# Kernel optimization log

Measured on AMD Instinct MI355X. Metric: run time of the kernel, lower is better.

## Reference

```python
import jax, jax.numpy as jnp
import numpy as np

D, H, L, FF, IN, OUT, S, B = 512, 8, 6, 2048, 32, 3, 512, 32


def setup_inputs() -> dict:
    key = jax.random.key(0)
    ks = iter(jax.random.split(key, 32))
    w = lambda shape: jax.random.normal(next(ks), shape, jnp.float32) * 0.02
    z = lambda shape: jnp.zeros(shape, jnp.float32)
    o = lambda shape: jnp.ones(shape, jnp.float32)
    return {
        'x': jax.random.normal(next(ks), (B, S, IN), jnp.float32),
        'w_in': w((IN, D)), 'b_in': z((D,)), 'g_in': o((D,)), 'be_in': z((D,)),
        'w_qkv': w((L, D, 3 * D)), 'b_qkv': z((L, 3 * D)),
        'w_out': w((L, D, D)), 'b_out': z((L, D)),
        'g1': o((L, D)), 'be1': z((L, D)),
        'w_ff1': w((L, D, FF)), 'b_ff1': z((L, FF)),
        'w_ff2': w((L, FF, D)), 'b_ff2': z((L, D)),
        'g2': o((L, D)), 'be2': z((L, D)),
        'w_h1': w((D, D // 2)), 'b_h1': z((D // 2,)),
        'w_h2': w((D // 2, OUT)), 'b_h2': z((OUT,)),
    }


def _layer_norm(x, g, b, eps=1e-5):
    mu = jnp.mean(x, axis=-1, keepdims=True)
    var = jnp.mean(jnp.square(x - mu), axis=-1, keepdims=True)
    return (x - mu) / jnp.sqrt(var + eps) * g + b


def _gelu(x):
    return jax.nn.gelu(x, approximate=False)  # torch nn.GELU default (erf)


def _pos_encoding(seq_len, d_model):
    pos = jnp.arange(seq_len, dtype=jnp.float32)[:, None]
    div = jnp.exp(jnp.arange(0, d_model, 2, dtype=jnp.float32) * (-np.log(10000.0) / d_model))
    pe = jnp.zeros((seq_len, d_model), jnp.float32)
    pe = pe.at[:, 0::2].set(jnp.sin(pos * div))
    pe = pe.at[:, 1::2].set(jnp.cos(pos * div))
    return pe


def reference(x, w_in, b_in, g_in, be_in, w_qkv, b_qkv, w_out, b_out,
              g1, be1, w_ff1, b_ff1, w_ff2, b_ff2, g2, be2,
              w_h1, b_h1, w_h2, b_h2):
    b, s, _ = x.shape
    d = w_in.shape[1]
    hd = d // H
    scale = hd ** -0.5

    # input projection: Linear -> LayerNorm -> GELU (dropout = identity at eval)
    h = _gelu(_layer_norm(x @ w_in + b_in, g_in, be_in))
    h = h + _pos_encoding(s, d)

    causal_mask = jnp.triu(jnp.ones((s, s), bool), 1)  # True above diagonal = future

    for l in range(w_qkv.shape[0]):
        qkv = (h @ w_qkv[l] + b_qkv[l]).reshape(b, s, 3, H, hd)
        q, k, v = qkv[:, :, 0], qkv[:, :, 1], qkv[:, :, 2]  # [b, s, H, hd]
        scores = jnp.einsum('bihd,bjhd->bhij', q, k) * scale
        scores = jnp.where(causal_mask, -jnp.inf, scores)
        attn = jax.nn.softmax(scores, axis=-1)
        o = jnp.einsum('bhij,bjhd->bihd', attn, v).reshape(b, s, d)
        o = o @ w_out[l] + b_out[l]
        h = _layer_norm(h + o, g1[l], be1[l])
        f = _gelu(h @ w_ff1[l] + b_ff1[l]) @ w_ff2[l] + b_ff2[l]
        h = _layer_norm(h + f, g2[l], be2[l])

    logits = _gelu(h @ w_h1 + b_h1) @ w_h2 + b_h2  # [b, s, OUT]
    return logits[:, -1, :]  # last position only
```

## Files before the change

### kernel.cpp

```cpp
#include <hip/hip_runtime.h>
#include <hip/hip_bf16.h>
#include <math.h>

#define D_   512
#define H_   8
#define HD_  64
#define L_   6
#define FF_  2048
#define IN_  32
#define OUT_ 3
#define S_   512
#define B_   32
#define M_   (B_ * S_)

typedef __attribute__((ext_vector_type(8))) short short8;
typedef __attribute__((ext_vector_type(4))) float floatx4;

__device__ __forceinline__ float gelu_f(float x) {
    const float ax = fabsf(x) * 0.70710678118654752f;
    const float t = __builtin_amdgcn_rcpf(fmaf(0.3275911f, ax, 1.0f));
    float p = fmaf(1.061405429f, t, -1.453152027f);
    p = fmaf(p, t, 1.421413741f);
    p = fmaf(p, t, -0.284496736f);
    p = fmaf(p, t, 0.254829592f);
    p = p * t;
    const float e = __expf(-ax * ax);
    const float er = copysignf(fmaf(-p, e, 1.0f), x);
    return 0.5f * x * (1.0f + er);
}
__device__ __forceinline__ float bf2f(unsigned short u) {
    union { unsigned int i; float f; } c; c.i = ((unsigned)u) << 16; return c.f;
}
__device__ __forceinline__ unsigned short f2bf(float v) {
    __hip_bfloat16 t = __float2bfloat16(v);
    return *(unsigned short*)&t;
}
__device__ __forceinline__ void async16(const void* g, void* l) {
    __builtin_amdgcn_global_load_lds(
        (const __attribute__((address_space(1))) unsigned int*)g,
        (__attribute__((address_space(3))) unsigned int*)l, 16, 0, 0);
}
__device__ __forceinline__ void stage2(const short* g, char* d, long rs, int off2) {
    async16(g, d);
    async16(g + rs, d + off2);
}


template<int DO_GELU, int OUT_BF16, int ADD_RES>
__global__ __launch_bounds__(256, 2)
void gemm_mfma_k(const __hip_bfloat16* __restrict__ A,
                 const __hip_bfloat16* __restrict__ WT,
                 const float* __restrict__ bias,
                 const float* __restrict__ R,
                 void* __restrict__ C,
                 int N, int K) {
    __shared__ __align__(16) char smem[65536];
    float* Ep = (float*)smem;

    const int tid  = threadIdx.x;
    const int lane = tid & 63;
    const int wave = tid >> 6;

    const int Lid = blockIdx.y * gridDim.x + blockIdx.x;
    const int xcd = Lid & 7;
    const int idx = Lid >> 3;
    const int gx  = gridDim.x, gy8 = gridDim.y >> 3;
    const int m0 = (xcd * gy8 + idx / gx) * 128;
    const int n0 = (idx % gx) * 128;

    const int wm = (wave >> 1) * 64, wn = (wave & 1) * 64;
    const int r = lane & 15, q = lane >> 4;
    const int qa = (q ^ ((r >> 1) & 3)) * 8;

    const int srow = tid >> 2;
    const int sc = ((tid & 3) ^ ((tid >> 3) & 3)) * 8;
    const short* Ag = (const short*)A + (long)(m0 + srow) * K + sc;
    const short* Bg = (const short*)WT + (long)(n0 + srow) * K + sc;
    const long rs = (long)64 * K;

    floatx4 acc[4][4];
    #pragma unroll
    for (int i = 0; i < 4; i++)
        #pragma unroll
        for (int j = 0; j < 4; j++) acc[i][j] = (floatx4)0.f;

    const int NT = K >> 6;

    stage2(Ag,      smem + 0     + tid * 16, rs, 4096);
    stage2(Bg,      smem + 16384 + tid * 16, rs, 4096);
    stage2(Ag + 32, smem + 8192  + tid * 16, rs, 4096);
    stage2(Bg + 32, smem + 24576 + tid * 16, rs, 4096);
    asm volatile("s_waitcnt vmcnt(4)" ::: "memory");
    __builtin_amdgcn_s_barrier();
    __builtin_amdgcn_sched_barrier(0);

    short8 a[4], b[4];
    for (int t = 0; t < NT; ++t) {
        const int cur = t & 1, nxt = cur ^ 1;
        const bool hn = (t + 1 < NT);
        const short* As = (const short*)(smem + cur * 32768);
        const short* Bs = (const short*)(smem + cur * 32768 + 16384);
        const short* Agt = Ag + (t + 1) * 64;
        const short* Bgt = Bg + (t + 1) * 64;
        char* Ad = smem + nxt * 32768;
        char* Bd = smem + nxt * 32768 + 16384;

        if (hn) {
            stage2(Agt, Ad + tid * 16, rs, 4096);
            stage2(Bgt, Bd + tid * 16, rs, 4096);
        }
        #pragma unroll
        for (int i = 0; i < 4; i++)
            a[i] = *(const short8*)&As[(wm + i * 16 + r) * 32 + qa];
        #pragma unroll
        for (int j = 0; j < 4; j++)
            b[j] = *(const short8*)&Bs[(wn + j * 16 + r) * 32 + qa];
        #pragma unroll
        for (int i = 0; i < 4; i++)
            #pragma unroll
            for (int j = 0; j < 4; j++)
                acc[i][j] = __builtin_amdgcn_mfma_f32_16x16x32_bf16(
                    a[i], b[j], acc[i][j], 0, 0, 0);
        __builtin_amdgcn_sched_barrier(0);
        if (hn) asm volatile("s_waitcnt vmcnt(4)" ::: "memory");
        else    asm volatile("s_waitcnt vmcnt(0)" ::: "memory");
        __builtin_amdgcn_s_barrier();
        __builtin_amdgcn_sched_barrier(0);

        if (hn) {
            stage2(Agt + 32, Ad + 8192 + tid * 16, rs, 4096);
            stage2(Bgt + 32, Bd + 8192 + tid * 16, rs, 4096);
        }
        #pragma unroll
        for (int i = 0; i < 4; i++)
            a[i] = *(const short8*)&As[4096 + (wm + i * 16 + r) * 32 + qa];
        #pragma unroll
        for (int j = 0; j < 4; j++)
            b[j] = *(const short8*)&Bs[4096 + (wn + j * 16 + r) * 32 + qa];
        #pragma unroll
        for (int i = 0; i < 4; i++)
            #pragma unroll
            for (int j = 0; j < 4; j++)
                acc[i][j] = __builtin_amdgcn_mfma_f32_16x16x32_bf16(
                    a[i], b[j], acc[i][j], 0, 0, 0);
        __builtin_amdgcn_sched_barrier(0);
        if (hn) asm volatile("s_waitcnt vmcnt(4)" ::: "memory");
        __builtin_amdgcn_s_barrier();
        __builtin_amdgcn_sched_barrier(0);
    }

    const int erow = tid >> 5;
    const int ecol = (tid & 31) * 4;
    const float4 bvec = *(const float4*)&bias[n0 + ecol];

    #pragma unroll
    for (int pass = 0; pass < 2; pass++) {
        if (pass) __syncthreads();
        if ((wave >> 1) == pass) {
            #pragma unroll
            for (int i = 0; i < 4; i++)
                #pragma unroll
                for (int j = 0; j < 4; j++)
                    #pragma unroll
                    for (int rg = 0; rg < 4; rg++)
                        Ep[(i * 16 + q * 4 + rg) * 132 + wn + j * 16 + r] =
                            acc[i][j][rg];
        }
        __syncthreads();
        #pragma unroll
        for (int it = 0; it < 8; it++) {
            const int row = it * 8 + erow;
            const long grow = (long)(m0 + pass * 64 + row) * N + n0 + ecol;
            const float4 v = *(const float4*)&Ep[row * 132 + ecol];
            float o0 = v.x + bvec.x, o1 = v.y + bvec.y;
            float o2 = v.z + bvec.z, o3 = v.w + bvec.w;
            if (DO_GELU) {
                o0 = gelu_f(o0); o1 = gelu_f(o1);
                o2 = gelu_f(o2); o3 = gelu_f(o3);
            }
            if (ADD_RES) {
                const float4 rv = *(const float4*)&R[grow];
                o0 += rv.x; o1 += rv.y; o2 += rv.z; o3 += rv.w;
            }
            if (OUT_BF16) {
                ushort4 pk;
                pk.x = f2bf(o0); pk.y = f2bf(o1);
                pk.z = f2bf(o2); pk.w = f2bf(o3);
                *(ushort4*)((unsigned short*)C + grow) = pk;
            } else {
                *(float4*)((float*)C + grow) = make_float4(o0, o1, o2, o3);
            }
        }
    }
}

__global__ __launch_bounds__(512, 1)
void gemm_ln_k(const __hip_bfloat16* __restrict__ A,
               const __hip_bfloat16* __restrict__ WT,
               const float* __restrict__ bias,
               const float* R,
               const float* __restrict__ g,
               const float* __restrict__ be,
               float* Hout,
               __hip_bfloat16* __restrict__ Hb,
               int K) {
    __shared__ __align__(16) char smem[147456];
    const int tid  = threadIdx.x;
    const int lane = tid & 63;
    const int wave = tid >> 6;

    const int Lid = blockIdx.x;
    const int m0 = ((Lid & 7) * 32 + (Lid >> 3)) * 64;

    const int r = lane & 15, q = lane >> 4;
    const int qaB  = (q ^ ((r >> 1) & 3)) * 8;
    const int qaA0 = ((q)     ^ (r & 7)) * 8;
    const int qaA1 = ((4 + q) ^ (r & 7)) * 8;
    const int wn = wave * 64;

    const int arow = tid >> 3;
    const int asb  = ((tid & 7) ^ ((tid >> 3) & 7)) * 8;
    const short* Ag = (const short*)A + (long)(m0 + arow) * K + asb;
    const int brow = tid >> 2;
    const int bsb  = ((tid & 3) ^ ((tid >> 3) & 3)) * 8;
    const short* Bg = (const short*)WT + (long)brow * K + bsb;
    const long brs = (long)128 * K;

    floatx4 acc[4][4];
    #pragma unroll
    for (int i = 0; i < 4; i++)
        #pragma unroll
        for (int j = 0; j < 4; j++) acc[i][j] = (floatx4)0.f;

    const int NTT = K >> 6;

    {
        char* base = smem;
        async16(Ag, base + tid * 16);
        const short* p0 = Bg;
        char* d0 = base + 8192 + tid * 16;
        async16(p0, d0); async16(p0 + brs, d0 + 8192);
        async16(p0 + 2 * brs, d0 + 16384); async16(p0 + 3 * brs, d0 + 24576);
        const short* p1 = Bg + 32;
        char* d1 = base + 40960 + tid * 16;
        async16(p1, d1); async16(p1 + brs, d1 + 8192);
        async16(p1 + 2 * brs, d1 + 16384); async16(p1 + 3 * brs, d1 + 24576);
    }
    asm volatile("s_waitcnt vmcnt(4)" ::: "memory");
    __builtin_amdgcn_s_barrier();
    __builtin_amdgcn_sched_barrier(0);

    for (int t = 0; t < NTT; ++t) {
        const int cur = t & 1, nxt = cur ^ 1;
        const bool hn = (t + 1 < NTT);
        const short* As  = (const short*)(smem + cur * 73728);
        const short* B0s = (const short*)(smem + cur * 73728 + 8192);
        const short* B1s = (const short*)(smem + cur * 73728 + 40960);
        char* nb = smem + nxt * 73728;
        const long k1 = (long)(t + 1) * 64;

        if (hn) {
            async16(Ag + k1, nb + tid * 16);
            const short* p0 = Bg + k1;
            char* d0 = nb + 8192 + tid * 16;
            async16(p0, d0); async16(p0 + brs, d0 + 8192);
            async16(p0 + 2 * brs, d0 + 16384); async16(p0 + 3 * brs, d0 + 24576);
        }
        {
            short8 a[4], b[4];
            #pragma unroll
            for (int mf = 0; mf < 4; mf++)
                a[mf] = *(const short8*)&As[(mf * 16 + r) * 64 + qaA0];
            #pragma unroll
            for (int nf = 0; nf < 4; nf++)
                b[nf] = *(const short8*)&B0s[(wn + nf * 16 + r) * 32 + qaB];
            #pragma unroll
            for (int mf = 0; mf < 4; mf++)
                #pragma unroll
                for (int nf = 0; nf < 4; nf++)
                    acc[mf][nf] = __builtin_amdgcn_mfma_f32_16x16x32_bf16(
                        a[mf], b[nf], acc[mf][nf], 0, 0, 0);
        }
        __builtin_amdgcn_sched_barrier(0);
        if (hn) asm volatile("s_waitcnt vmcnt(4)" ::: "memory");
        else    asm volatile("s_waitcnt vmcnt(0)" ::: "memory");
        __builtin_amdgcn_s_barrier();
        __builtin_amdgcn_sched_barrier(0);

        if (hn) {
            const short* p1 = Bg + k1 + 32;
            char* d1 = nb + 40960 + tid * 16;
            async16(p1, d1); async16(p1 + brs, d1 + 8192);
            async16(p1 + 2 * brs, d1 + 16384); async16(p1 + 3 * brs, d1 + 24576);
        }
        {
            short8 a[4], b[4];
            #pragma unroll
            for (int mf = 0; mf < 4; mf++)
                a[mf] = *(const short8*)&As[(mf * 16 + r) * 64 + qaA1];
            #pragma unroll
            for (int nf = 0; nf < 4; nf++)
                b[nf] = *(const short8*)&B1s[(wn + nf * 16 + r) * 32 + qaB];
            #pragma unroll
            for (int mf = 0; mf < 4; mf++)
                #pragma unroll
                for (int nf = 0; nf < 4; nf++)
                    acc[mf][nf] = __builtin_amdgcn_mfma_f32_16x16x32_bf16(
                        a[mf], b[nf], acc[mf][nf], 0, 0, 0);
        }
        __builtin_amdgcn_sched_barrier(0);
        if (hn) asm volatile("s_waitcnt vmcnt(4)" ::: "memory");
        __builtin_amdgcn_s_barrier();
        __builtin_amdgcn_sched_barrier(0);
    }

    float* Ef = (float*)smem;
    float* stat = (float*)(smem + 132096);
    const float gl = g[tid], bl = be[tid], bv = bias[tid];

    #pragma unroll
    for (int mf = 0; mf < 4; mf++)
        #pragma unroll
        for (int nf = 0; nf < 4; nf++)
            #pragma unroll
            for (int rg = 0; rg < 4; rg++)
                Ef[(mf * 16 + q * 4 + rg) * 516 + wn + nf * 16 + r] =
                    acc[mf][nf][rg];
    __syncthreads();
    #pragma unroll 8
    for (int k = 0; k < 64; k++)
        Ef[k * 516 + tid] += bv + R[(long)(m0 + k) * 512 + tid];
    __syncthreads();
    {
        const int row = tid >> 3, cc = tid & 7;
        float s = 0.f, ss = 0.f;
        #pragma unroll 8
        for (int j = 0; j < 64; j++) {
            const float v = Ef[row * 516 + cc + 8 * j];
            s += v; ss += v * v;
        }
        #pragma unroll
        for (int off = 1; off < 8; off <<= 1) {
            s  += __shfl_xor(s, off);
            ss += __shfl_xor(ss, off);
        }
        const float mu  = s * (1.0f / 512.0f);
        const float var = fmaxf(ss * (1.0f / 512.0f) - mu * mu, 0.f);
        const float inv = 1.0f / sqrtf(var + 1e-5f);
        if (cc == 0) { stat[row * 2] = mu; stat[row * 2 + 1] = inv; }
    }
    __syncthreads();
    #pragma unroll 8
    for (int k = 0; k < 64; k++) {
        const float v  = Ef[k * 516 + tid];
        const float o  = (v - stat[k * 2]) * stat[k * 2 + 1] * gl + bl;
        const long idx = (long)(m0 + k) * 512 + tid;
        Hout[idx] = o;
        ((unsigned short*)Hb)[idx] = f2bf(o);
    }
}

__global__ __launch_bounds__(256)
void transpose_cast_k(const float* __restrict__ W, __hip_bfloat16* __restrict__ WT,
                      int K, int N) {
    __shared__ float tile[32][33];
    const float* Wl = W + (long)blockIdx.z * K * N;
    __hip_bfloat16* WTl = WT + (long)blockIdx.z * K * N;
    const int n0 = blockIdx.x * 32, k0 = blockIdx.y * 32;
    const int tx = threadIdx.x & 31, ty = threadIdx.x >> 5;
    for (int rr = ty; rr < 32; rr += 8)
        tile[rr][tx] = Wl[(long)(k0 + rr) * N + n0 + tx];
    __syncthreads();
    for (int rr = ty; rr < 32; rr += 8)
        WTl[(long)(n0 + rr) * K + k0 + tx] = __float2bfloat16(tile[tx][rr]);
}

template<int DO_GELU>
__global__ __launch_bounds__(256)
void gemm_bias_k(const float* __restrict__ A, long lda,
                 const float* __restrict__ W,
                 const float* __restrict__ bias,
                 float* __restrict__ C,
                 int M, int N, int K) {
    __shared__ float As[16][64];
    __shared__ float Ws[16][64];
    const int tx = threadIdx.x;
    const int ty = threadIdx.y;
    const int tid = ty * 16 + tx;
    const int m0 = blockIdx.y * 64;
    const int n0 = blockIdx.x * 64;
    float acc[4][4] = {};
    for (int k0 = 0; k0 < K; k0 += 16) {
        #pragma unroll
        for (int e = tid; e < 64 * 16; e += 256) {
            int m = e >> 4, k = e & 15;
            float v = 0.f;
            if (m0 + m < M) v = A[(long)(m0 + m) * lda + k0 + k];
            As[k][m] = v;
        }
        #pragma unroll
        for (int e = tid; e < 16 * 64; e += 256) {
            int k = e >> 6, n = e & 63;
            float v = 0.f;
            if (n0 + n < N) v = W[(long)(k0 + k) * N + n0 + n];
            Ws[k][n] = v;
        }
        __syncthreads();
        #pragma unroll
        for (int kk = 0; kk < 16; kk++) {
            float a[4], w[4];
            #pragma unroll
            for (int i = 0; i < 4; i++) a[i] = As[kk][ty * 4 + i];
            #pragma unroll
            for (int j = 0; j < 4; j++) w[j] = Ws[kk][tx * 4 + j];
            #pragma unroll
            for (int i = 0; i < 4; i++)
                #pragma unroll
                for (int j = 0; j < 4; j++)
                    acc[i][j] += a[i] * w[j];
        }
        __syncthreads();
    }
    #pragma unroll
    for (int i = 0; i < 4; i++) {
        int m = m0 + ty * 4 + i;
        if (m >= M) continue;
        #pragma unroll
        for (int j = 0; j < 4; j++) {
            int n = n0 + tx * 4 + j;
            if (n >= N) continue;
            float v = acc[i][j] + bias[n];
            if (DO_GELU) v = gelu_f(v);
            C[(long)m * N + n] = v;
        }
    }
}

__global__ __launch_bounds__(256)
void ln_gelu_pos_k(const float* __restrict__ X,
                   const float* __restrict__ g,
                   const float* __restrict__ be,
                   float* __restrict__ Hout,
                   __hip_bfloat16* __restrict__ Hb) {
    const int row = blockIdx.x;
    const int s = row & (S_ - 1);
    const int t = threadIdx.x;
    const float* x = X + (long)row * D_;
    float v0 = x[t], v1 = x[t + 256];
    __shared__ float red[256];
    red[t] = v0 + v1;
    __syncthreads();
    for (int off = 128; off; off >>= 1) {
        if (t < off) red[t] += red[t + off];
        __syncthreads();
    }
    float mu = red[0] * (1.0f / D_);
    __syncthreads();
    float d0 = v0 - mu, d1 = v1 - mu;
    red[t] = d0 * d0 + d1 * d1;
    __syncthreads();
    for (int off = 128; off; off >>= 1) {
        if (t < off) red[t] += red[t + off];
        __syncthreads();
    }
    float var = red[0] * (1.0f / D_);
    float inv = 1.0f / sqrtf(var + 1e-5f);
    float o0 = gelu_f(d0 * inv * g[t] + be[t]);
    float o1 = gelu_f(d1 * inv * g[t + 256] + be[t + 256]);
    {
        int d = t, i = d >> 1;
        float dv = expf((float)(2 * i) * (-9.210340371976184f / 512.0f));
        float ang = (float)s * dv;
        o0 += (d & 1) ? cosf(ang) : sinf(ang);
    }
    {
        int d = t + 256, i = d >> 1;
        float dv = expf((float)(2 * i) * (-9.210340371976184f / 512.0f));
        float ang = (float)s * dv;
        o1 += (d & 1) ? cosf(ang) : sinf(ang);
    }
    Hout[(long)row * D_ + t] = o0;
    Hout[(long)row * D_ + t + 256] = o1;
    Hb[(long)row * D_ + t] = __float2bfloat16(o0);
    Hb[(long)row * D_ + t + 256] = __float2bfloat16(o1);
}

#define LDT 72
__global__ __launch_bounds__(256)
void attn_mfma_k(const __hip_bfloat16* __restrict__ qkv,
                 __hip_bfloat16* __restrict__ O) {
    const int qt = blockIdx.x;
    const int bh = blockIdx.y;
    const int b = bh >> 3, h = bh & (H_ - 1);
    const int tid = threadIdx.x;
    const int wave = tid >> 6, lane = tid & 63;
    const int ln = lane & 15, quad = lane >> 4;
    const int wm = wave * 32;
    const int i0 = qt * 128;

    __shared__ unsigned short Qs[128 * LDT];
    __shared__ unsigned short Ks[64 * LDT];
    __shared__ unsigned short Vt[64 * LDT];
    __shared__ unsigned short Ps[128 * LDT];
    __shared__ float stat[128];

    const unsigned short* base = (const unsigned short*)qkv + (long)b * S_ * (3 * D_);

    {
        const int r0 = tid >> 3, c0 = (tid & 7) * 8;
        #pragma unroll
        for (int i = 0; i < 4; i++) {
            const int rw = i * 32 + r0;
            *(short8*)&Qs[rw * LDT + c0] =
                *(const short8*)(base + (long)(i0 + rw) * (3 * D_) + h * HD_ + c0);
        }
    }

    float m_i[2] = { -INFINITY, -INFINITY };
    float l_i[2] = { 0.f, 0.f };
    floatx4 o_acc[2][4];
    #pragma unroll
    for (int i = 0; i < 2; i++)
        #pragma unroll
        for (int j = 0; j < 4; j++) o_acc[i][j] = (floatx4)0.f;

    const int kr = tid >> 2, kc = (tid & 3) * 16;
    const int vj = tid & 63, vc = (tid >> 6) * 16;

    const int ktmax = 2 * qt + 1;
    for (int kt = 0; kt <= ktmax; kt++) {
        const int j0 = kt * 64;
        {
            const unsigned short* kp = base + (long)(j0 + kr) * (3 * D_) + D_ + h * HD_ + kc;
            *(short8*)&Ks[kr * LDT + kc]     = *(const short8*)(kp);
            *(short8*)&Ks[kr * LDT + kc + 8] = *(const short8*)(kp + 8);
            const unsigned short* vp = base + (long)(j0 + vj) * (3 * D_) + 2 * D_ + h * HD_ + vc;
            short8 v0 = *(const short8*)(vp);
            short8 v1 = *(const short8*)(vp + 8);
            #pragma unroll
            for (int e = 0; e < 8; e++) {
                Vt[(vc + e) * LDT + vj]     = (unsigned short)v0[e];
                Vt[(vc + 8 + e) * LDT + vj] = (unsigned short)v1[e];
            }
        }
        __syncthreads();

        floatx4 sa[4][2];
        #pragma unroll
        for (int mt = 0; mt < 4; mt++)
            #pragma unroll
            for (int nt = 0; nt < 2; nt++) sa[mt][nt] = (floatx4)0.f;
        #pragma unroll
        for (int c = 0; c < 2; c++) {
            short8 kf[4], qf[2];
            #pragma unroll
            for (int mt = 0; mt < 4; mt++)
                kf[mt] = *(const short8*)&Ks[(mt * 16 + ln) * LDT + c * 32 + quad * 8];
            #pragma unroll
            for (int nt = 0; nt < 2; nt++)
                qf[nt] = *(const short8*)&Qs[(wm + nt * 16 + ln) * LDT + c * 32 + quad * 8];
            #pragma unroll
            for (int mt = 0; mt < 4; mt++)
                #pragma unroll
                for (int nt = 0; nt < 2; nt++)
                    sa[mt][nt] = __builtin_amdgcn_mfma_f32_16x16x32_bf16(
                        kf[mt], qf[nt], sa[mt][nt], 0, 0, 0);
        }

        const bool domask = (kt >= 2 * qt);
        #pragma unroll
        for (int nt = 0; nt < 2; nt++) {
            const int qg = i0 + wm + nt * 16 + ln;
            float mx = -INFINITY;
            #pragma unroll
            for (int mt = 0; mt < 4; mt++)
                #pragma unroll
                for (int rg = 0; rg < 4; rg++) {
                    float v = sa[mt][nt][rg] * 0.125f;
                    if (domask && (j0 + mt * 16 + quad * 4 + rg > qg)) v = -INFINITY;
                    sa[mt][nt][rg] = v;
                    mx = fmaxf(mx, v);
                }
            mx = fmaxf(mx, __shfl_xor(mx, 16));
            mx = fmaxf(mx, __shfl_xor(mx, 32));
            const float mn = fmaxf(m_i[nt], mx);
            const float alpha = __expf(m_i[nt] - mn);
            m_i[nt] = mn;
            float ls = 0.f;
            #pragma unroll
            for (int mt = 0; mt < 4; mt++) {
                ushort4 pk;
                float p0 = __expf(sa[mt][nt][0] - mn);
                float p1 = __expf(sa[mt][nt][1] - mn);
                float p2 = __expf(sa[mt][nt][2] - mn);
                float p3 = __expf(sa[mt][nt][3] - mn);
                ls += p0 + p1 + p2 + p3;
                pk.x = f2bf(p0); pk.y = f2bf(p1); pk.z = f2bf(p2); pk.w = f2bf(p3);
                *(ushort4*)&Ps[(wm + nt * 16 + ln) * LDT + mt * 16 + quad * 4] = pk;
            }
            ls += __shfl_xor(ls, 16);
            ls += __shfl_xor(ls, 32);
            l_i[nt] = l_i[nt] * alpha + ls;
            if (quad == 0) stat[wm + nt * 16 + ln] = alpha;
        }

        #pragma unroll
        for (int mt2 = 0; mt2 < 2; mt2++) {
            #pragma unroll
            for (int rg = 0; rg < 4; rg++) {
                const float a = stat[wm + mt2 * 16 + quad * 4 + rg];
                #pragma unroll
                for (int nt = 0; nt < 4; nt++) o_acc[mt2][nt][rg] *= a;
            }
        }

        #pragma unroll
        for (int c = 0; c < 2; c++) {
            short8 pf[2], vf[4];
            #pragma unroll
            for (int mt2 = 0; mt2 < 2; mt2++)
                pf[mt2] = *(const short8*)&Ps[(wm + mt2 * 16 + ln) * LDT + c * 32 + quad * 8];
            #pragma unroll
            for (int nt = 0; nt < 4; nt++)
                vf[nt] = *(const short8*)&Vt[(nt * 16 + ln) * LDT + c * 32 + quad * 8];
            #pragma unroll
            for (int mt2 = 0; mt2 < 2; mt2++)
                #pragma unroll
                for (int nt = 0; nt < 4; nt++)
                    o_acc[mt2][nt] = __builtin_amdgcn_mfma_f32_16x16x32_bf16(
                        pf[mt2], vf[nt], o_acc[mt2][nt], 0, 0, 0);
        }
        __syncthreads();
    }

    if (quad == 0) {
        stat[wm + ln]      = l_i[0];
        stat[wm + 16 + ln] = l_i[1];
    }
    unsigned short* Og = (unsigned short*)O;
    #pragma unroll
    for (int mt2 = 0; mt2 < 2; mt2++) {
        #pragma unroll
        for (int rg = 0; rg < 4; rg++) {
            const float linv = 1.0f / stat[wm + mt2 * 16 + quad * 4 + rg];
            const long row = (long)(b * S_ + i0 + wm + mt2 * 16 + quad * 4 + rg);
            #pragma unroll
            for (int nt = 0; nt < 4; nt++)
                Og[row * D_ + h * HD_ + nt * 16 + ln] =
                    f2bf(o_acc[mt2][nt][rg] * linv);
        }
    }
}

__global__ __launch_bounds__(256)
void head1_k(const float* __restrict__ h, const float* __restrict__ w1,
             const float* __restrict__ b1, float* __restrict__ th) {
    __shared__ float hs[D_];
    const int b = blockIdx.x, n = threadIdx.x;
    const float* hr = h + (long)(b * S_ + S_ - 1) * D_;
    hs[n] = hr[n];
    hs[n + 256] = hr[n + 256];
    __syncthreads();
    float s = 0.f;
    #pragma unroll 8
    for (int k = 0; k < D_; k++) s += hs[k] * w1[(long)k * 256 + n];
    th[b * 256 + n] = gelu_f(s + b1[n]);
}

__global__ __launch_bounds__(64)
void head2_k(const float* __restrict__ th, const float* __restrict__ w2,
             const float* __restrict__ b2, float* __restrict__ out) {
    const int b = blockIdx.x, lane = threadIdx.x;
    const float* t = th + b * 256;
    float s0 = 0.f, s1 = 0.f, s2 = 0.f;
    #pragma unroll
    for (int e = 0; e < 4; e++) {
        const int k = lane * 4 + e;
        const float tv = t[k];
        s0 += tv * w2[k * 3 + 0];
        s1 += tv * w2[k * 3 + 1];
        s2 += tv * w2[k * 3 + 2];
    }
    #pragma unroll
    for (int off = 1; off < 64; off <<= 1) {
        s0 += __shfl_xor(s0, off);
        s1 += __shfl_xor(s1, off);
        s2 += __shfl_xor(s2, off);
    }
    if (lane == 0) {
        out[b * 3 + 0] = s0 + b2[0];
        out[b * 3 + 1] = s1 + b2[1];
        out[b * 3 + 2] = s2 + b2[2];
    }
}

extern "C" void kernel_launch(void* const* d_in, const int* in_sizes, int n_in,
                              void* d_out, int out_size, void* d_ws, size_t ws_size,
                              hipStream_t stream) {
    const float* x     = (const float*)d_in[0];
    const float* w_in  = (const float*)d_in[1];
    const float* b_in  = (const float*)d_in[2];
    const float* g_in  = (const float*)d_in[3];
    const float* be_in = (const float*)d_in[4];
    const float* w_qkv = (const float*)d_in[5];
    const float* b_qkv = (const float*)d_in[6];
    const float* w_out = (const float*)d_in[7];
    const float* b_out = (const float*)d_in[8];
    const float* g1    = (const float*)d_in[9];
    const float* be1   = (const float*)d_in[10];
    const float* w_ff1 = (const float*)d_in[11];
    const float* b_ff1 = (const float*)d_in[12];
    const float* w_ff2 = (const float*)d_in[13];
    const float* b_ff2 = (const float*)d_in[14];
    const float* g2    = (const float*)d_in[15];
    const float* be2   = (const float*)d_in[16];
    const float* w_h1  = (const float*)d_in[17];
    const float* b_h1  = (const float*)d_in[18];
    const float* w_h2  = (const float*)d_in[19];
    const float* b_h2  = (const float*)d_in[20];
    float* out = (float*)d_out;

    float* h    = (float*)d_ws;
    float* bufB = h + (long)M_ * D_;
    float* th   = bufB + (long)M_ * D_;
    __hip_bfloat16* hb    = (__hip_bfloat16*)(th + 32 * 256);
    __hip_bfloat16* attb  = hb + (long)M_ * D_;
    __hip_bfloat16* bufAb = attb + (long)M_ * D_;
    __hip_bfloat16* qkvT  = bufAb + (long)M_ * FF_;
    __hip_bfloat16* outT  = qkvT + (long)L_ * (3 * D_) * D_;
    __hip_bfloat16* ff1T  = outT + (long)L_ * D_ * D_;
    __hip_bfloat16* ff2T  = ff1T + (long)L_ * FF_ * D_;

    dim3 blk(16, 16);

    transpose_cast_k<<<dim3((3 * D_) / 32, D_ / 32, L_), 256, 0, stream>>>(w_qkv, qkvT, D_, 3 * D_);
    transpose_cast_k<<<dim3(D_ / 32, D_ / 32, L_), 256, 0, stream>>>(w_out, outT, D_, D_);
    transpose_cast_k<<<dim3(FF_ / 32, D_ / 32, L_), 256, 0, stream>>>(w_ff1, ff1T, D_, FF_);
    transpose_cast_k<<<dim3(D_ / 32, FF_ / 32, L_), 256, 0, stream>>>(w_ff2, ff2T, FF_, D_);

    gemm_bias_k<0><<<dim3(D_ / 64, M_ / 64), blk, 0, stream>>>(
        x, IN_, w_in, b_in, bufB, M_, D_, IN_);
    ln_gelu_pos_k<<<M_, 256, 0, stream>>>(bufB, g_in, be_in, h, hb);

    for (int l = 0; l < L_; l++) {
        gemm_mfma_k<0, 1, 0><<<dim3((3 * D_) / 128, M_ / 128), 256, 0, stream>>>(
            hb, qkvT + (long)l * (3 * D_) * D_, b_qkv + l * 3 * D_, nullptr,
            bufAb, 3 * D_, D_);
        attn_mfma_k<<<dim3(S_ / 128, B_ * H_), 256, 0, stream>>>(bufAb, attb);
        gemm_ln_k<<<256, 512, 0, stream>>>(
            attb, outT + (long)l * D_ * D_, b_out + l * D_, h,
            g1 + l * D_, be1 + l * D_, h, hb, D_);
        gemm_mfma_k<1, 1, 0><<<dim3(FF_ / 128, M_ / 128), 256, 0, stream>>>(
            hb, ff1T + (long)l * FF_ * D_, b_ff1 + l * FF_, nullptr,
            bufAb, FF_, D_);
        gemm_ln_k<<<256, 512, 0, stream>>>(
            bufAb, ff2T + (long)l * D_ * FF_, b_ff2 + l * D_, h,
            g2 + l * D_, be2 + l * D_, h, hb, FF_);
    }

    head1_k<<<B_, 256, 0, stream>>>(h, w_h1, b_h1, th);
    head2_k<<<B_, 64, 0, stream>>>(th, w_h2, b_h2, out);
}
```

Measured before the change: 1.592 ms.

## Triple-buffer A tiles in gemm_ln kernel to prefetch two steps ahead

Reworks the shared-memory pipeline of the fused GEMM+LayerNorm kernel. A tiles now use a three-slot ring buffer and are prefetched two K-steps ahead, while B tiles stay double-buffered. Tail iterations issue redundant clamped loads so every wait can use a uniform vmcnt(5), with a final vmcnt(0) drain after the loop. This aims to hide more global-load latency for A, at the cost of more LDS (155648 bytes), redundant loads at the tail, and a longer in-flight load queue.

```diff
diff --git a/kernel.cpp b/kernel.cpp
--- a/kernel.cpp
+++ b/kernel.cpp
@@ -204,7 +204,7 @@
                float* Hout,
                __hip_bfloat16* __restrict__ Hb,
                int K) {
-    __shared__ __align__(16) char smem[147456];
+    __shared__ __align__(16) char smem[155648];
     const int tid  = threadIdx.x;
     const int lane = tid & 63;
     const int wave = tid >> 6;
@@ -235,36 +235,37 @@
     const int NTT = K >> 6;
 
     {
-        char* base = smem;
-        async16(Ag, base + tid * 16);
         const short* p0 = Bg;
-        char* d0 = base + 8192 + tid * 16;
+        char* d0 = smem + 24576 + tid * 16;
         async16(p0, d0); async16(p0 + brs, d0 + 8192);
         async16(p0 + 2 * brs, d0 + 16384); async16(p0 + 3 * brs, d0 + 24576);
+        async16(Ag, smem + tid * 16);
+        const int t1 = (1 < NTT) ? 1 : (NTT - 1);
+        async16(Ag + (long)t1 * 64, smem + 8192 + tid * 16);
         const short* p1 = Bg + 32;
-        char* d1 = base + 40960 + tid * 16;
+        char* d1 = smem + 24576 + 32768 + tid * 16;
         async16(p1, d1); async16(p1 + brs, d1 + 8192);
         async16(p1 + 2 * brs, d1 + 16384); async16(p1 + 3 * brs, d1 + 24576);
     }
-    asm volatile("s_waitcnt vmcnt(4)" ::: "memory");
+    asm volatile("s_waitcnt vmcnt(5)" ::: "memory");
     __builtin_amdgcn_s_barrier();
     __builtin_amdgcn_sched_barrier(0);
 
+    int slotR = 0;
     for (int t = 0; t < NTT; ++t) {
-        const int cur = t & 1, nxt = cur ^ 1;
-        const bool hn = (t + 1 < NTT);
-        const short* As  = (const short*)(smem + cur * 73728);
-        const short* B0s = (const short*)(smem + cur * 73728 + 8192);
-        const short* B1s = (const short*)(smem + cur * 73728 + 40960);
-        char* nb = smem + nxt * 73728;
-        const long k1 = (long)(t + 1) * 64;
-
-        if (hn) {
-            async16(Ag + k1, nb + tid * 16);
-            const short* p0 = Bg + k1;
-            char* d0 = nb + 8192 + tid * 16;
+        const short* As  = (const short*)(smem + slotR * 8192);
+        const short* B0s = (const short*)(smem + 24576 + (t & 1) * 65536);
+        const short* B1s = B0s + 16384;
+        const int tp1 = (t + 1 < NTT) ? t + 1 : NTT - 1;
+        const int tp2 = (t + 2 < NTT) ? t + 2 : NTT - 1;
+        int slotW = slotR + 2; if (slotW >= 3) slotW -= 3;
+
+        {
+            const short* p0 = Bg + (long)tp1 * 64;
+            char* d0 = smem + 24576 + ((t + 1) & 1) * 65536 + tid * 16;
             async16(p0, d0); async16(p0 + brs, d0 + 8192);
             async16(p0 + 2 * brs, d0 + 16384); async16(p0 + 3 * brs, d0 + 24576);
+            async16(Ag + (long)tp2 * 64, smem + slotW * 8192 + tid * 16);
         }
         {
             short8 a[4], b[4];
@@ -282,14 +283,13 @@
                         a[mf], b[nf], acc[mf][nf], 0, 0, 0);
         }
         __builtin_amdgcn_sched_barrier(0);
-        if (hn) asm volatile("s_waitcnt vmcnt(4)" ::: "memory");
-        else    asm volatile("s_waitcnt vmcnt(0)" ::: "memory");
+        asm volatile("s_waitcnt vmcnt(5)" ::: "memory");
         __builtin_amdgcn_s_barrier();
         __builtin_amdgcn_sched_barrier(0);
 
-        if (hn) {
-            const short* p1 = Bg + k1 + 32;
-            char* d1 = nb + 40960 + tid * 16;
+        {
+            const short* p1 = Bg + (long)tp1 * 64 + 32;
+            char* d1 = smem + 24576 + ((t + 1) & 1) * 65536 + 32768 + tid * 16;
             async16(p1, d1); async16(p1 + brs, d1 + 8192);
             async16(p1 + 2 * brs, d1 + 16384); async16(p1 + 3 * brs, d1 + 24576);
         }
@@ -309,10 +309,16 @@
                         a[mf], b[nf], acc[mf][nf], 0, 0, 0);
         }
         __builtin_amdgcn_sched_barrier(0);
-        if (hn) asm volatile("s_waitcnt vmcnt(4)" ::: "memory");
+        asm volatile("s_waitcnt vmcnt(5)" ::: "memory");
         __builtin_amdgcn_s_barrier();
         __builtin_amdgcn_sched_barrier(0);
-    }
+
+        slotR = slotR + 1; if (slotR >= 3) slotR -= 3;
+    }
+
+    asm volatile("s_waitcnt vmcnt(0)" ::: "memory");
+    __builtin_amdgcn_s_barrier();
+    __builtin_amdgcn_sched_barrier(0);
 
     float* Ef = (float*)smem;
     float* stat = (float*)(smem + 132096);
```

After: 1.600 ms (median of 2 runs). About the same (+0.5%).

## Shrink gemm_ln LDS footprint with 32-wide K steps to raise occupancy

Applied to the files above, without the earlier changes.

Rewrites the fused GEMM+LayerNorm kernel to step K in 32-element slices. The B tile is double-buffered per slice, and the A tile is prefetched two slices at a time split across thread halves. LDS drops from 144KB to 80KB, and the epilogue runs in two 32-row chunks so the smaller buffer is enough. Launch bounds go from 1 to 4 blocks per CU, to allow more resident blocks and better latency hiding. Separately, the sched_barrier fences are removed from the plain GEMM kernel so the compiler can interleave instructions. The cost is twice as many barriers per K and some redundant clamped loads at the tail.

```diff
diff --git a/kernel.cpp b/kernel.cpp
--- a/kernel.cpp
+++ b/kernel.cpp
@@ -92,7 +92,6 @@
     stage2(Bg + 32, smem + 24576 + tid * 16, rs, 4096);
     asm volatile("s_waitcnt vmcnt(4)" ::: "memory");
     __builtin_amdgcn_s_barrier();
-    __builtin_amdgcn_sched_barrier(0);
 
     short8 a[4], b[4];
     for (int t = 0; t < NT; ++t) {
@@ -121,11 +120,9 @@
             for (int j = 0; j < 4; j++)
                 acc[i][j] = __builtin_amdgcn_mfma_f32_16x16x32_bf16(
                     a[i], b[j], acc[i][j], 0, 0, 0);
-        __builtin_amdgcn_sched_barrier(0);
         if (hn) asm volatile("s_waitcnt vmcnt(4)" ::: "memory");
         else    asm volatile("s_waitcnt vmcnt(0)" ::: "memory");
         __builtin_amdgcn_s_barrier();
-        __builtin_amdgcn_sched_barrier(0);
 
         if (hn) {
             stage2(Agt + 32, Ad + 8192 + tid * 16, rs, 4096);
@@ -143,10 +140,8 @@
             for (int j = 0; j < 4; j++)
                 acc[i][j] = __builtin_amdgcn_mfma_f32_16x16x32_bf16(
                     a[i], b[j], acc[i][j], 0, 0, 0);
-        __builtin_amdgcn_sched_barrier(0);
         if (hn) asm volatile("s_waitcnt vmcnt(4)" ::: "memory");
         __builtin_amdgcn_s_barrier();
-        __builtin_amdgcn_sched_barrier(0);
     }
 
     const int erow = tid >> 5;
@@ -194,7 +189,7 @@
     }
 }
 
-__global__ __launch_bounds__(512, 1)
+__global__ __launch_bounds__(512, 4)
 void gemm_ln_k(const __hip_bfloat16* __restrict__ A,
                const __hip_bfloat16* __restrict__ WT,
                const float* __restrict__ bias,
@@ -204,7 +199,7 @@
                float* Hout,
                __hip_bfloat16* __restrict__ Hb,
                int K) {
-    __shared__ __align__(16) char smem[147456];
+    __shared__ __align__(16) char smem[81920];
     const int tid  = threadIdx.x;
     const int lane = tid & 63;
     const int wave = tid >> 6;
@@ -213,150 +208,124 @@
     const int m0 = ((Lid & 7) * 32 + (Lid >> 3)) * 64;
 
     const int r = lane & 15, q = lane >> 4;
-    const int qaB  = (q ^ ((r >> 1) & 3)) * 8;
-    const int qaA0 = ((q)     ^ (r & 7)) * 8;
-    const int qaA1 = ((4 + q) ^ (r & 7)) * 8;
+    const int qa = (q ^ ((r >> 1) & 3)) * 8;
     const int wn = wave * 64;
 
-    const int arow = tid >> 3;
-    const int asb  = ((tid & 7) ^ ((tid >> 3) & 7)) * 8;
-    const short* Ag = (const short*)A + (long)(m0 + arow) * K + asb;
     const int brow = tid >> 2;
     const int bsb  = ((tid & 3) ^ ((tid >> 3) & 3)) * 8;
     const short* Bg = (const short*)WT + (long)brow * K + bsb;
     const long brs = (long)128 * K;
 
+    const int ahalf  = tid >> 8;
+    const int alocal = tid & 255;
+    const int arow   = alocal >> 2;
+    const int asb    = ((alocal & 3) ^ ((alocal >> 3) & 3)) * 8;
+    const short* Ag  = (const short*)A + (long)(m0 + arow) * K + asb;
+
     floatx4 acc[4][4];
     #pragma unroll
     for (int i = 0; i < 4; i++)
         #pragma unroll
         for (int j = 0; j < 4; j++) acc[i][j] = (floatx4)0.f;
 
-    const int NTT = K >> 6;
+    const int NTT = K >> 5;
 
     {
-        char* base = smem;
-        async16(Ag, base + tid * 16);
-        const short* p0 = Bg;
-        char* d0 = base + 8192 + tid * 16;
-        async16(p0, d0); async16(p0 + brs, d0 + 8192);
-        async16(p0 + 2 * brs, d0 + 16384); async16(p0 + 3 * brs, d0 + 24576);
-        const short* p1 = Bg + 32;
-        char* d1 = base + 40960 + tid * 16;
-        async16(p1, d1); async16(p1 + brs, d1 + 8192);
-        async16(p1 + 2 * brs, d1 + 16384); async16(p1 + 3 * brs, d1 + 24576);
-    }
-    asm volatile("s_waitcnt vmcnt(4)" ::: "memory");
+        char* d0 = smem + 16384 + tid * 16;
+        async16(Bg, d0); async16(Bg + brs, d0 + 8192);
+        async16(Bg + 2 * brs, d0 + 16384); async16(Bg + 3 * brs, d0 + 24576);
+        const int ka = (ahalf < NTT) ? ahalf : NTT - 1;
+        async16(Ag + (long)ka * 32, smem + tid * 16);
+    }
+    asm volatile("s_waitcnt vmcnt(0)" ::: "memory");
     __builtin_amdgcn_s_barrier();
-    __builtin_amdgcn_sched_barrier(0);
 
     for (int t = 0; t < NTT; ++t) {
-        const int cur = t & 1, nxt = cur ^ 1;
-        const bool hn = (t + 1 < NTT);
-        const short* As  = (const short*)(smem + cur * 73728);
-        const short* B0s = (const short*)(smem + cur * 73728 + 8192);
-        const short* B1s = (const short*)(smem + cur * 73728 + 40960);
-        char* nb = smem + nxt * 73728;
-        const long k1 = (long)(t + 1) * 64;
-
-        if (hn) {
-            async16(Ag + k1, nb + tid * 16);
-            const short* p0 = Bg + k1;
-            char* d0 = nb + 8192 + tid * 16;
-            async16(p0, d0); async16(p0 + brs, d0 + 8192);
-            async16(p0 + 2 * brs, d0 + 16384); async16(p0 + 3 * brs, d0 + 24576);
-        }
         {
-            short8 a[4], b[4];
-            #pragma unroll
-            for (int mf = 0; mf < 4; mf++)
-                a[mf] = *(const short8*)&As[(mf * 16 + r) * 64 + qaA0];
+            const int kb = (t + 1 < NTT) ? t + 1 : NTT - 1;
+            const short* p = Bg + (long)kb * 32;
+            char* d = smem + 16384 + ((t + 1) & 1) * 32768 + tid * 16;
+            async16(p, d); async16(p + brs, d + 8192);
+            async16(p + 2 * brs, d + 16384); async16(p + 3 * brs, d + 24576);
+        }
+        if (!(t & 1)) {
+            const int kt = t + 2 + ahalf;
+            const int ka = (kt < NTT) ? kt : NTT - 1;
+            async16(Ag + (long)ka * 32,
+                    smem + (((t >> 1) + 1) & 1) * 8192 + tid * 16);
+        }
+        const short* As = (const short*)(smem + ((t >> 1) & 1) * 8192 +
+                                         (t & 1) * 4096);
+        const short* Bs = (const short*)(smem + 16384 + (t & 1) * 32768);
+        short8 a[4], b[4];
+        #pragma unroll
+        for (int mf = 0; mf < 4; mf++)
+            a[mf] = *(const short8*)&As[(mf * 16 + r) * 32 + qa];
+        #pragma unroll
+        for (int nf = 0; nf < 4; nf++)
+            b[nf] = *(const short8*)&Bs[(wn + nf * 16 + r) * 32 + qa];
+        #pragma unroll
+        for (int mf = 0; mf < 4; mf++)
             #pragma unroll
             for (int nf = 0; nf < 4; nf++)
-                b[nf] = *(const short8*)&B0s[(wn + nf * 16 + r) * 32 + qaB];
-            #pragma unroll
-            for (int mf = 0; mf < 4; mf++)
+                acc[mf][nf] = __builtin_amdgcn_mfma_f32_16x16x32_bf16(
+                    a[mf], b[nf], acc[mf][nf], 0, 0, 0);
+        if (!(t & 1)) asm volatile("s_waitcnt vmcnt(1)" ::: "memory");
+        else          asm volatile("s_waitcnt vmcnt(0)" ::: "memory");
+        __builtin_amdgcn_s_barrier();
+    }
+
+    asm volatile("s_waitcnt vmcnt(0)" ::: "memory");
+    __builtin_amdgcn_s_barrier();
+
+    float* Ef = (float*)smem;
+    float* stat = (float*)(smem + 66048);
+    const float gl = g[tid], bl = be[tid], bv = bias[tid];
+
+    #pragma unroll
+    for (int ch = 0; ch < 2; ch++) {
+        if (ch) __syncthreads();
+        #pragma unroll
+        for (int m2 = 0; m2 < 2; m2++)
+            #pragma unroll
+            for (int nf = 0; nf < 4; nf++)
                 #pragma unroll
-                for (int nf = 0; nf < 4; nf++)
-                    acc[mf][nf] = __builtin_amdgcn_mfma_f32_16x16x32_bf16(
-                        a[mf], b[nf], acc[mf][nf], 0, 0, 0);
-        }
-        __builtin_amdgcn_sched_barrier(0);
-        if (hn) asm volatile("s_waitcnt vmcnt(4)" ::: "memory");
-        else    asm volatile("s_waitcnt vmcnt(0)" ::: "memory");
-        __builtin_amdgcn_s_barrier();
-        __builtin_amdgcn_sched_barrier(0);
-
-        if (hn) {
-            const short* p1 = Bg + k1 + 32;
-            char* d1 = nb + 40960 + tid * 16;
-            async16(p1, d1); async16(p1 + brs, d1 + 8192);
-            async16(p1 + 2 * brs, d1 + 16384); async16(p1 + 3 * brs, d1 + 24576);
-        }
+                for (int rg = 0; rg < 4; rg++)
+                    Ef[(m2 * 16 + q * 4 + rg) * 516 + wn + nf * 16 + r] =
+                        acc[2 * ch + m2][nf][rg];
+        __syncthreads();
+        const int gm = m0 + ch * 32;
+        #pragma unroll 8
+        for (int k = 0; k < 32; k++)
+            Ef[k * 516 + tid] += bv + R[(long)(gm + k) * 512 + tid];
+        __syncthreads();
         {
-            short8 a[4], b[4];
-            #pragma unroll
-            for (int mf = 0; mf < 4; mf++)
-                a[mf] = *(const short8*)&As[(mf * 16 + r) * 64 + qaA1];
-            #pragma unroll
-            for (int nf = 0; nf < 4; nf++)
-                b[nf] = *(const short8*)&B1s[(wn + nf * 16 + r) * 32 + qaB];
-            #pragma unroll
-            for (int mf = 0; mf < 4; mf++)
-                #pragma unroll
-                for (int nf = 0; nf < 4; nf++)
-                    acc[mf][nf] = __builtin_amdgcn_mfma_f32_16x16x32_bf16(
-                        a[mf], b[nf], acc[mf][nf], 0, 0, 0);
-        }
-        __builtin_amdgcn_sched_barrier(0);
-        if (hn) asm volatile("s_waitcnt vmcnt(4)" ::: "memory");
-        __builtin_amdgcn_s_barrier();
-        __builtin_amdgcn_sched_barrier(0);
-    }
-
-    float* Ef = (float*)smem;
-    float* stat = (float*)(smem + 132096);
-    const float gl = g[tid], bl = be[tid], bv = bias[tid];
-
-    #pragma unroll
-    for (int mf = 0; mf < 4; mf++)
-        #pragma unroll
-        for (int nf = 0; nf < 4; nf++)
-            #pragma unroll
-            for (int rg = 0; rg < 4; rg++)
-                Ef[(mf * 16 + q * 4 + rg) * 516 + wn + nf * 16 + r] =
-                    acc[mf][nf][rg];
-    __syncthreads();
-    #pragma unroll 8
-    for (int k = 0; k < 64; k++)
-        Ef[k * 516 + tid] += bv + R[(long)(m0 + k) * 512 + tid];
-    __syncthreads();
-    {
-        const int row = tid >> 3, cc = tid & 7;
-        float s = 0.f, ss = 0.f;
+            const int row = tid >> 4, cc = tid & 15;
+            float s = 0.f, ss = 0.f;
+            #pragma unroll 8
+            for (int j = 0; j < 32; j++) {
+                const float v = Ef[row * 516 + cc + 16 * j];
+                s += v; ss += v * v;
+            }
+            #pragma unroll
+            for (int off = 1; off < 16; off <<= 1) {
+                s  += __shfl_xor(s, off);
+                ss += __shfl_xor(ss, off);
+            }
+            const float mu  = s * (1.0f / 512.0f);
+            const float var = fmaxf(ss * (1.0f / 512.0f) - mu * mu, 0.f);
+            const float inv = 1.0f / sqrtf(var + 1e-5f);
+            if (cc == 0) { stat[row * 2] = mu; stat[row * 2 + 1] = inv; }
+        }
+        __syncthreads();
         #pragma unroll 8
-        for (int j = 0; j < 64; j++) {
-            const float v = Ef[row * 516 + cc + 8 * j];
-            s += v; ss += v * v;
-        }
-        #pragma unroll
-        for (int off = 1; off < 8; off <<= 1) {
-            s  += __shfl_xor(s, off);
-            ss += __shfl_xor(ss, off);
-        }
-        const float mu  = s * (1.0f / 512.0f);
-        const float var = fmaxf(ss * (1.0f / 512.0f) - mu * mu, 0.f);
-        const float inv = 1.0f / sqrtf(var + 1e-5f);
-        if (cc == 0) { stat[row * 2] = mu; stat[row * 2 + 1] = inv; }
-    }
-    __syncthreads();
-    #pragma unroll 8
-    for (int k = 0; k < 64; k++) {
-        const float v  = Ef[k * 516 + tid];
-        const float o  = (v - stat[k * 2]) * stat[k * 2 + 1] * gl + bl;
-        const long idx = (long)(m0 + k) * 512 + tid;
-        Hout[idx] = o;
-        ((unsigned short*)Hb)[idx] = f2bf(o);
+        for (int k = 0; k < 32; k++) {
+            const float v  = Ef[k * 516 + tid];
+            const float o  = (v - stat[k * 2]) * stat[k * 2 + 1] * gl + bl;
+            const long idx = (long)(gm + k) * 512 + tid;
+            Hout[idx] = o;
+            ((unsigned short*)Hb)[idx] = f2bf(o);
+        }
     }
 }
 
```

Result: slower. 1.717 ms (+7.8%).
